# Kernel optimization log

Hardware: AMD Instinct MI355X
Metric: run time of the kernel (lower is better)

## Reference

```python
import jax, jax.numpy as jnp
import numpy as np

TOTAL_NODES = 10000
E_OLD = 320000
E_NEW = 320000


def setup_inputs() -> dict:
    key = jax.random.key(0)
    k1, k2, k3, k4, k5 = jax.random.split(key, 5)
    edge_index_old = jax.random.randint(k1, (2, E_OLD), 0, TOTAL_NODES, dtype=jnp.int32)
    # Make new edges overlap old edges for half of E_new so both the
    # retained-edge and new-edge branches are exercised.
    rand_new = jax.random.randint(k2, (2, E_NEW), 0, TOTAL_NODES, dtype=jnp.int32)
    half = E_NEW // 2
    edge_index_new = jnp.concatenate([edge_index_old[:, :half], rand_new[:, half:]], axis=1)
    edge_attr_old = jax.random.normal(k3, (E_OLD, 3), dtype=jnp.float32)
    flow_old = jax.random.normal(k4, (E_OLD, 1), dtype=jnp.float32)
    edge_attr_new = jax.random.normal(k5, (E_NEW, 3), dtype=jnp.float32)
    return {
        "edge_index_old": edge_index_old,
        "edge_attr_old": edge_attr_old,
        "flow_old": flow_old,
        "edge_index_new": edge_index_new,
        "edge_attr_new": edge_attr_new,
        "total_nodes": TOTAL_NODES,
    }


def reference(edge_index_old, edge_attr_old, flow_old, edge_index_new, edge_attr_new, total_nodes):
    dtype = edge_attr_new.dtype
    E_old = edge_attr_old.shape[0]
    # key(src, dst) = src * total_nodes + dst  (unique per node pair)
    old_keys = edge_index_old[0] * total_nodes + edge_index_old[1]  # [E_old] int32
    new_keys = edge_index_new[0] * total_nodes + edge_index_new[1]  # [E_new] int32
    # Dense scatter-built lookup table of size total_nodes^2 (the memory hog).
    table = jnp.full((total_nodes * total_nodes,), -1, dtype=jnp.int32)
    table = table.at[old_keys].set(jnp.arange(E_old, dtype=jnp.int32))
    match_idx = table[new_keys]                    # [E_new], -1 if no match
    retained = match_idx >= 0                      # [E_new] bool
    old_feats = jnp.concatenate([edge_attr_old, flow_old], axis=-1)  # [E_old, 4]
    gathered = old_feats[jnp.where(retained, match_idx, 0)]          # [E_new, 4]
    aligned_old = jnp.where(retained[:, None], gathered, jnp.zeros((), dtype=dtype))
    is_new_edge = (~retained).astype(dtype)[:, None]                 # [E_new, 1]
    return jnp.concatenate([aligned_old, edge_attr_new, is_new_edge], axis=-1)  # [E_new, 8]
```

## Files before the change

kernel.cpp:

```cpp
#include <hip/hip_runtime.h>


#define EMPTY_SLOT 0xAAAAAAAAAAAAAAAAull
#define EMPTY_KEY  0xAAAAAAAAu

typedef float vfloat4 __attribute__((ext_vector_type(4)));

__device__ __forceinline__ unsigned hash_key(unsigned key, unsigned mask) {
    unsigned h = key * 2654435761u;
    h ^= h >> 16;
    return h & mask;
}

__global__ void __launch_bounds__(512)
insert_kernel(const int* __restrict__ ei_old, int E_old,
              const float* __restrict__ attr_old,
              const float* __restrict__ flow_old,
              const int* __restrict__ total_nodes_p,
              unsigned long long* __restrict__ slots,
              vfloat4* __restrict__ feats,
              unsigned mask) {
    int e = blockIdx.x * blockDim.x + threadIdx.x;
    if (e >= E_old) return;

    vfloat4 f;
    f.x = __builtin_nontemporal_load(&attr_old[3 * e + 0]);
    f.y = __builtin_nontemporal_load(&attr_old[3 * e + 1]);
    f.z = __builtin_nontemporal_load(&attr_old[3 * e + 2]);
    f.w = __builtin_nontemporal_load(&flow_old[e]);
    feats[e] = f;

    const int tn  = *total_nodes_p;
    const int src = __builtin_nontemporal_load(&ei_old[e]);
    const int dst = __builtin_nontemporal_load(&ei_old[E_old + e]);
    const unsigned key = (unsigned)(src * tn + dst);
    const unsigned long long desired =
        ((unsigned long long)(unsigned)e << 32) | key;

    unsigned h = hash_key(key, mask);
    for (;;) {
        unsigned long long old = atomicCAS(&slots[h], EMPTY_SLOT, desired);
        if (old == EMPTY_SLOT) return;
        if ((unsigned)old == key) {
            atomicMax(&slots[h], desired);
            return;
        }
        h = (h + 1) & mask;
    }
}

__global__ void __launch_bounds__(512)
align_kernel(const int* __restrict__ ei_new, int E_new,
             const vfloat4* __restrict__ feats,
             const float* __restrict__ attr_new,
             const int* __restrict__ total_nodes_p,
             const unsigned long long* __restrict__ slots,
             unsigned mask, float* __restrict__ out) {
    int e = blockIdx.x * blockDim.x + threadIdx.x;
    if (e >= E_new) return;
    const int tn  = *total_nodes_p;
    const int src = __builtin_nontemporal_load(&ei_new[e]);
    const int dst = __builtin_nontemporal_load(&ei_new[E_new + e]);
    const unsigned key = (unsigned)(src * tn + dst);

    unsigned h = hash_key(key, mask);
    int m = -1;
    for (;;) {
        unsigned long long cur = slots[h];
        unsigned ck = (unsigned)cur;
        if (ck == key) { m = (int)(cur >> 32); break; }
        if (ck == EMPTY_KEY) break;
        h = (h + 1) & mask;
    }

    vfloat4 a, b;
    if (m >= 0) {
        a = feats[m];
        b.w = 0.0f;
    } else {
        a = (vfloat4){0.f, 0.f, 0.f, 0.f};
        b.w = 1.0f;
    }
    b.x = __builtin_nontemporal_load(&attr_new[3 * e + 0]);
    b.y = __builtin_nontemporal_load(&attr_new[3 * e + 1]);
    b.z = __builtin_nontemporal_load(&attr_new[3 * e + 2]);

    vfloat4* o = (vfloat4*)(out + 8 * (size_t)e);
    __builtin_nontemporal_store(a, &o[0]);
    __builtin_nontemporal_store(b, &o[1]);
}

extern "C" void kernel_launch(void* const* d_in, const int* in_sizes, int n_in,
                              void* d_out, int out_size, void* d_ws, size_t ws_size,
                              hipStream_t stream) {
    const int*   ei_old   = (const int*)  d_in[0];
    const float* attr_old = (const float*)d_in[1];
    const float* flow_old = (const float*)d_in[2];
    const int*   ei_new   = (const int*)  d_in[3];
    const float* attr_new = (const float*)d_in[4];
    const int*   tn_p     = (const int*)  d_in[5];

    const int E_old = in_sizes[0] / 2;
    const int E_new = in_sizes[3] / 2;

    size_t slots_n = 1u << 20;
    while (slots_n * 8 + (size_t)E_old * 16 > ws_size && slots_n > (1u << 19))
        slots_n >>= 1;
    unsigned mask = (unsigned)slots_n - 1;

    unsigned long long* slots = (unsigned long long*)d_ws;
    vfloat4* feats = (vfloat4*)((char*)d_ws + slots_n * 8);

    const int B = 512;
    insert_kernel<<<(E_old + B - 1) / B, B, 0, stream>>>(
        ei_old, E_old, attr_old, flow_old, tn_p, slots, feats, mask);
    align_kernel<<<(E_new + B - 1) / B, B, 0, stream>>>(
        ei_new, E_new, feats, attr_new, tn_p, slots, mask, (float*)d_out);
}
```

Before: 105.7 us.

## Fuse insert and align into one cooperative kernel with grid sync

```diff
diff --git a/kernel.cpp b/kernel.cpp
--- a/kernel.cpp
+++ b/kernel.cpp
@@ -1,10 +1,15 @@
 #include <hip/hip_runtime.h>
+#include <hip/hip_cooperative_groups.h>
+
+namespace cg = cooperative_groups;
 
 
 #define EMPTY_SLOT 0xAAAAAAAAAAAAAAAAull
 #define EMPTY_KEY  0xAAAAAAAAu
 
 typedef float vfloat4 __attribute__((ext_vector_type(4)));
+typedef float vfloat2 __attribute__((ext_vector_type(2)));
+typedef int   vint2   __attribute__((ext_vector_type(2)));
 
 __device__ __forceinline__ unsigned hash_key(unsigned key, unsigned mask) {
     unsigned h = key * 2654435761u;
@@ -12,82 +17,158 @@
     return h & mask;
 }
 
-__global__ void __launch_bounds__(512)
-insert_kernel(const int* __restrict__ ei_old, int E_old,
-              const float* __restrict__ attr_old,
-              const float* __restrict__ flow_old,
-              const int* __restrict__ total_nodes_p,
-              unsigned long long* __restrict__ slots,
-              vfloat4* __restrict__ feats,
-              unsigned mask) {
-    int e = blockIdx.x * blockDim.x + threadIdx.x;
-    if (e >= E_old) return;
-
-    vfloat4 f;
-    f.x = __builtin_nontemporal_load(&attr_old[3 * e + 0]);
-    f.y = __builtin_nontemporal_load(&attr_old[3 * e + 1]);
-    f.z = __builtin_nontemporal_load(&attr_old[3 * e + 2]);
-    f.w = __builtin_nontemporal_load(&flow_old[e]);
-    feats[e] = f;
-
-    const int tn  = *total_nodes_p;
-    const int src = __builtin_nontemporal_load(&ei_old[e]);
-    const int dst = __builtin_nontemporal_load(&ei_old[E_old + e]);
-    const unsigned key = (unsigned)(src * tn + dst);
-    const unsigned long long desired =
-        ((unsigned long long)(unsigned)e << 32) | key;
-
+__device__ __forceinline__ void insert_one(unsigned key, unsigned idx,
+                                           unsigned long long* __restrict__ slots,
+                                           unsigned mask) {
+    const unsigned long long des = ((unsigned long long)idx << 32) | key;
     unsigned h = hash_key(key, mask);
     for (;;) {
-        unsigned long long old = atomicCAS(&slots[h], EMPTY_SLOT, desired);
+        const unsigned long long old = atomicCAS(&slots[h], EMPTY_SLOT, des);
         if (old == EMPTY_SLOT) return;
         if ((unsigned)old == key) {
-            atomicMax(&slots[h], desired);
+            atomicMax(&slots[h], des);
             return;
         }
         h = (h + 1) & mask;
     }
 }
 
-__global__ void __launch_bounds__(512)
-align_kernel(const int* __restrict__ ei_new, int E_new,
-             const vfloat4* __restrict__ feats,
+__device__ __forceinline__ int resolve_probe(unsigned long long cur,
+                                             unsigned key, unsigned h,
+                                             const unsigned long long* __restrict__ slots,
+                                             unsigned mask) {
+    for (;;) {
+        const unsigned ck = (unsigned)cur;
+        if (ck == key) return (int)(cur >> 32);
+        if (ck == EMPTY_KEY) return -1;
+        h = (h + 1) & mask;
+        cur = slots[h];
+    }
+}
+
+__global__ void __launch_bounds__(256, 4)
+fused_kernel(const int* __restrict__ ei_old, int E_old,
+             const float* __restrict__ attr_old,
+             const float* __restrict__ flow_old,
+             const int* __restrict__ ei_new, int E_new,
              const float* __restrict__ attr_new,
-             const int* __restrict__ total_nodes_p,
-             const unsigned long long* __restrict__ slots,
-             unsigned mask, float* __restrict__ out) {
-    int e = blockIdx.x * blockDim.x + threadIdx.x;
-    if (e >= E_new) return;
-    const int tn  = *total_nodes_p;
-    const int src = __builtin_nontemporal_load(&ei_new[e]);
-    const int dst = __builtin_nontemporal_load(&ei_new[E_new + e]);
-    const unsigned key = (unsigned)(src * tn + dst);
-
-    unsigned h = hash_key(key, mask);
-    int m = -1;
-    for (;;) {
-        unsigned long long cur = slots[h];
-        unsigned ck = (unsigned)cur;
-        if (ck == key) { m = (int)(cur >> 32); break; }
-        if (ck == EMPTY_KEY) break;
-        h = (h + 1) & mask;
-    }
-
-    vfloat4 a, b;
-    if (m >= 0) {
-        a = feats[m];
-        b.w = 0.0f;
-    } else {
-        a = (vfloat4){0.f, 0.f, 0.f, 0.f};
-        b.w = 1.0f;
-    }
-    b.x = __builtin_nontemporal_load(&attr_new[3 * e + 0]);
-    b.y = __builtin_nontemporal_load(&attr_new[3 * e + 1]);
-    b.z = __builtin_nontemporal_load(&attr_new[3 * e + 2]);
-
-    vfloat4* o = (vfloat4*)(out + 8 * (size_t)e);
-    __builtin_nontemporal_store(a, &o[0]);
-    __builtin_nontemporal_store(b, &o[1]);
+             const int* __restrict__ tn_p,
+             unsigned long long* __restrict__ slots,
+             unsigned mask,
+             float* __restrict__ out) {
+    const int t    = blockIdx.x * blockDim.x + threadIdx.x;
+    const int nthr = gridDim.x * blockDim.x;
+    const int tn   = *tn_p;
+
+    for (int e = t; e < E_old; e += nthr) {
+        const int src = __builtin_nontemporal_load(ei_old + e);
+        const int dst = __builtin_nontemporal_load(ei_old + E_old + e);
+        insert_one((unsigned)(src * tn + dst), (unsigned)e, slots, mask);
+    }
+
+    const int  n0   = 2 * t;
+    const bool pair = (n0 + 1 < E_new);
+    const bool tail = (n0 + 1 == E_new);
+    vint2   sv = {0, 0};
+    int     d0 = 0, d1 = 0;
+    vfloat2 a0 = {0.f, 0.f}, a1 = {0.f, 0.f}, a2 = {0.f, 0.f};
+    if (pair) {
+        sv = __builtin_nontemporal_load((const vint2*)(ei_new + n0));
+        d0 = __builtin_nontemporal_load(ei_new + E_new + n0);
+        d1 = __builtin_nontemporal_load(ei_new + E_new + n0 + 1);
+        a0 = __builtin_nontemporal_load((const vfloat2*)(attr_new + 3 * n0));
+        a1 = __builtin_nontemporal_load((const vfloat2*)(attr_new + 3 * n0 + 2));
+        a2 = __builtin_nontemporal_load((const vfloat2*)(attr_new + 3 * n0 + 4));
+    } else if (tail) {
+        sv.x = __builtin_nontemporal_load(ei_new + n0);
+        d0   = __builtin_nontemporal_load(ei_new + E_new + n0);
+        a0.x = __builtin_nontemporal_load(attr_new + 3 * n0);
+        a0.y = __builtin_nontemporal_load(attr_new + 3 * n0 + 1);
+        a1.x = __builtin_nontemporal_load(attr_new + 3 * n0 + 2);
+    }
+
+    cg::this_grid().sync();
+
+    if (pair) {
+        const unsigned key0 = (unsigned)(sv.x * tn + d0);
+        const unsigned key1 = (unsigned)(sv.y * tn + d1);
+        unsigned h0 = hash_key(key0, mask);
+        unsigned h1 = hash_key(key1, mask);
+        const unsigned long long c0 = slots[h0];
+        const unsigned long long c1 = slots[h1];
+        const int m0 = resolve_probe(c0, key0, h0, slots, mask);
+        const int m1 = resolve_probe(c1, key1, h1, slots, mask);
+
+        vfloat4 x0 = {0.f, 0.f, 0.f, 0.f};
+        vfloat4 x1 = {0.f, 0.f, 0.f, 0.f};
+        float f0 = 1.0f, f1 = 1.0f;
+        if (m0 >= 0) {
+            x0.x = attr_old[3 * m0];
+            x0.y = attr_old[3 * m0 + 1];
+            x0.z = attr_old[3 * m0 + 2];
+            x0.w = flow_old[m0];
+            f0 = 0.0f;
+        }
+        if (m1 >= 0) {
+            x1.x = attr_old[3 * m1];
+            x1.y = attr_old[3 * m1 + 1];
+            x1.z = attr_old[3 * m1 + 2];
+            x1.w = flow_old[m1];
+            f1 = 0.0f;
+        }
+        const vfloat4 y0 = {a0.x, a0.y, a1.x, f0};
+        const vfloat4 y1 = {a1.y, a2.x, a2.y, f1};
+        vfloat4* o = (vfloat4*)(out + 8 * (size_t)n0);
+        __builtin_nontemporal_store(x0, &o[0]);
+        __builtin_nontemporal_store(y0, &o[1]);
+        __builtin_nontemporal_store(x1, &o[2]);
+        __builtin_nontemporal_store(y1, &o[3]);
+    } else if (tail) {
+        const unsigned key = (unsigned)(sv.x * tn + d0);
+        unsigned h = hash_key(key, mask);
+        const int m = resolve_probe(slots[h], key, h, slots, mask);
+        vfloat4 x = {0.f, 0.f, 0.f, 0.f};
+        float fl = 1.0f;
+        if (m >= 0) {
+            x.x = attr_old[3 * m];
+            x.y = attr_old[3 * m + 1];
+            x.z = attr_old[3 * m + 2];
+            x.w = flow_old[m];
+            fl = 0.0f;
+        }
+        const vfloat4 y = {a0.x, a0.y, a1.x, fl};
+        vfloat4* o = (vfloat4*)(out + 8 * (size_t)n0);
+        __builtin_nontemporal_store(x, &o[0]);
+        __builtin_nontemporal_store(y, &o[1]);
+    }
+
+    for (int p = t + nthr; 2 * p < E_new; p += nthr) {
+        const int e0 = 2 * p;
+        for (int e = e0; e < e0 + 2 && e < E_new; ++e) {
+            const int src = ei_new[e];
+            const int dst = ei_new[E_new + e];
+            const unsigned key = (unsigned)(src * tn + dst);
+            unsigned h = hash_key(key, mask);
+            const int m = resolve_probe(slots[h], key, h, slots, mask);
+            vfloat4 x = {0.f, 0.f, 0.f, 0.f};
+            float fl = 1.0f;
+            if (m >= 0) {
+                x.x = attr_old[3 * m];
+                x.y = attr_old[3 * m + 1];
+                x.z = attr_old[3 * m + 2];
+                x.w = flow_old[m];
+                fl = 0.0f;
+            }
+            vfloat4 y;
+            y.x = attr_new[3 * e];
+            y.y = attr_new[3 * e + 1];
+            y.z = attr_new[3 * e + 2];
+            y.w = fl;
+            vfloat4* o = (vfloat4*)(out + 8 * (size_t)e);
+            __builtin_nontemporal_store(x, &o[0]);
+            __builtin_nontemporal_store(y, &o[1]);
+        }
+    }
 }
 
 extern "C" void kernel_launch(void* const* d_in, const int* in_sizes, int n_in,
@@ -100,20 +181,26 @@
     const float* attr_new = (const float*)d_in[4];
     const int*   tn_p     = (const int*)  d_in[5];
 
-    const int E_old = in_sizes[0] / 2;
-    const int E_new = in_sizes[3] / 2;
+    int E_old = in_sizes[0] / 2;
+    int E_new = in_sizes[3] / 2;
 
     size_t slots_n = 1u << 20;
-    while (slots_n * 8 + (size_t)E_old * 16 > ws_size && slots_n > (1u << 19))
-        slots_n >>= 1;
+    while (slots_n * 8 > ws_size && slots_n > (1u << 16)) slots_n >>= 1;
     unsigned mask = (unsigned)slots_n - 1;
-
     unsigned long long* slots = (unsigned long long*)d_ws;
-    vfloat4* feats = (vfloat4*)((char*)d_ws + slots_n * 8);
-
-    const int B = 512;
-    insert_kernel<<<(E_old + B - 1) / B, B, 0, stream>>>(
-        ei_old, E_old, attr_old, flow_old, tn_p, slots, feats, mask);
-    align_kernel<<<(E_new + B - 1) / B, B, 0, stream>>>(
-        ei_new, E_new, feats, attr_new, tn_p, slots, mask, (float*)d_out);
-}
+    float* outp = (float*)d_out;
+
+    const int B = 256;
+    int pairs  = (E_new + 1) / 2;
+    int blocks = (pairs + B - 1) / B;
+    if (blocks > 1024) blocks = 1024;
+    if (blocks < 1)    blocks = 1;
+
+    void* args[] = {
+        (void*)&ei_old, (void*)&E_old, (void*)&attr_old, (void*)&flow_old,
+        (void*)&ei_new, (void*)&E_new, (void*)&attr_new, (void*)&tn_p,
+        (void*)&slots,  (void*)&mask,  (void*)&outp,
+    };
+    hipLaunchCooperativeKernel((void*)fused_kernel, dim3(blocks), dim3(B),
+                               args, 0, stream);
+}
```

Result: slower. 185.7 us (+75.6%).
